# Optimization experiments

Hardware: AMD Instinct MI355X
Metric: run time of the kernel (lower is better)

The kernel has to match this reference:

```python
import jax, jax.numpy as jnp
import numpy as np

B, S, D_IN = 2, 2048, 2048
H, G, HD = 16, 4, 128          # heads, kv groups, head_dim
GS = H // G                    # group size (heads per kv group)
EPS = 1e-6
SCALE = HD ** -0.5


def rms_norm(x, w):
    # RMSNorm over last dim (head_dim)
    var = jnp.mean(jnp.square(x), axis=-1, keepdims=True)
    return x * jax.lax.rsqrt(var + EPS) * w


def apply_rope(x, cos, sin):
    # x: [b, h, s, d]; cos/sin: [s, d]. Rotate-half convention.
    d = x.shape[-1]
    x1, x2 = x[..., : d // 2], x[..., d // 2 :]
    rotated = jnp.concatenate([-x2, x1], axis=-1)
    return x * cos[None, None] + rotated * sin[None, None]


def setup_inputs() -> dict:
    key = jax.random.key(0)
    ks = jax.random.split(key, 8)
    x = jax.random.normal(ks[0], (B, S, D_IN), jnp.float32)
    mask = jnp.triu(jnp.ones((S, S), jnp.bool_), k=1)  # True = masked (future)
    # realistic RoPE tables
    inv_freq = 1.0 / (10000.0 ** (jnp.arange(0, HD, 2, dtype=jnp.float32) / HD))
    angles = jnp.arange(S, dtype=jnp.float32)[:, None] * inv_freq[None, :]  # [S, HD/2]
    angles = jnp.concatenate([angles, angles], axis=-1)  # [S, HD]
    cos, sin = jnp.cos(angles), jnp.sin(angles)
    sd = 0.02
    Wq = jax.random.normal(ks[1], (D_IN, H * HD), jnp.float32) * sd
    Wk = jax.random.normal(ks[2], (D_IN, G * HD), jnp.float32) * sd
    Wv = jax.random.normal(ks[3], (D_IN, G * HD), jnp.float32) * sd
    Wo = jax.random.normal(ks[4], (H * HD, D_IN), jnp.float32) * sd
    q_norm_w = jnp.ones((HD,), jnp.float32)
    k_norm_w = jnp.ones((HD,), jnp.float32)
    return {"x": x, "mask": mask, "cos": cos, "sin": sin, "Wq": Wq, "Wk": Wk,
            "Wv": Wv, "Wo": Wo, "q_norm_w": q_norm_w, "k_norm_w": k_norm_w}


def reference(x, mask, cos, sin, Wq, Wk, Wv, Wo, q_norm_w, k_norm_w):
    b, s, _ = x.shape
    q = (x @ Wq).reshape(b, s, H, HD).transpose(0, 2, 1, 3)   # [b,H,s,d]
    k = (x @ Wk).reshape(b, s, G, HD).transpose(0, 2, 1, 3)   # [b,G,s,d]
    v = (x @ Wv).reshape(b, s, G, HD).transpose(0, 2, 1, 3)   # [b,G,s,d]
    q = rms_norm(q, q_norm_w)
    k = rms_norm(k, k_norm_w)
    q = apply_rope(q, cos, sin)
    k = apply_rope(k, cos, sin)
    q = q * SCALE
    # GQA without materializing repeated KV: split heads into [G, GS]
    qg = q.reshape(b, G, GS, s, HD)                           # [b,G,gs,s,d]
    scores = jnp.einsum('bghsd,bgtd->bghst', qg, k)           # [b,G,gs,s,s]
    scores = jnp.where(mask[None, None, None], -jnp.inf, scores)
    attn = jax.nn.softmax(scores, axis=-1)
    ctx = jnp.einsum('bghst,bgtd->bghsd', attn, v)            # [b,G,gs,s,d]
    ctx = ctx.reshape(b, H, s, HD).transpose(0, 2, 1, 3).reshape(b, s, H * HD)
    return ctx @ Wo
```

## Files before the change

### kernel.cpp

```cpp
#include <hip/hip_runtime.h>
#include <cstdint>
#include <cstddef>

typedef unsigned short u16;
typedef __bf16 bf16x8 __attribute__((ext_vector_type(8)));
typedef float f32x4 __attribute__((ext_vector_type(4)));

#define SLEN 2048
#define NHEADS 16
#define NGRP 4

__device__ inline float bf2f(u16 u) { return __uint_as_float(((unsigned)u) << 16); }
__device__ inline u16 f2bf(float f) {
    unsigned u = __float_as_uint(f);
    u += 0x7fffu + ((u >> 16) & 1u);
    return (u16)(u >> 16);
}

__device__ inline f32x4 mfma16(bf16x8 a, bf16x8 b, f32x4 c) {
    return __builtin_amdgcn_mfma_f32_16x16x32_bf16(a, b, c, 0, 0, 0);
}

__device__ inline void memfence_compiler() { __asm__ volatile("" ::: "memory"); }

__device__ inline void cp16(const u16* g, u16* l) {
    __builtin_amdgcn_global_load_lds(
        (__attribute__((address_space(1))) void*)(u16*)g,
        (__attribute__((address_space(3))) void*)l, 16, 0, 0);
}


__device__ inline void transpose_f32_body(u16 (*tile)[65], const float* __restrict__ in,
                                          u16* __restrict__ out, int R, int C, int bx, int by,
                                          int tid) {
    const long r0 = (long)by * 64, c0 = (long)bx * 64;
    for (int j = 0; j < 4; j++) {
        int c = j * 256 + tid;
        int lr = c >> 4, lc = (c & 15) * 4;
        float4 v = *(const float4*)&in[(r0 + lr) * (long)C + c0 + lc];
        tile[lr][lc + 0] = f2bf(v.x); tile[lr][lc + 1] = f2bf(v.y);
        tile[lr][lc + 2] = f2bf(v.z); tile[lr][lc + 3] = f2bf(v.w);
    }
    __syncthreads();
    for (int j = 0; j < 4; j++) {
        int c = j * 256 + tid;
        int orow = c >> 4, oc = (c & 15) * 4;
        ushort4 vv;
        vv.x = tile[oc + 0][orow]; vv.y = tile[oc + 1][orow];
        vv.z = tile[oc + 2][orow]; vv.w = tile[oc + 3][orow];
        *(ushort4*)&out[(c0 + orow) * (long)R + r0 + oc] = vv;
    }
}

__device__ inline void transpose_bf_body(u16 (*tile)[65], const u16* __restrict__ in, long inRS,
                                         u16* __restrict__ out, int R, int C, int bx, int by,
                                         int tid) {
    const long r0 = (long)by * 64, c0 = (long)bx * 64;
    for (int j = 0; j < 4; j++) {
        int c = j * 256 + tid;
        int lr = c >> 4, lc = (c & 15) * 4;
        ushort4 vv = *(const ushort4*)&in[(r0 + lr) * inRS + c0 + lc];
        tile[lr][lc + 0] = vv.x; tile[lr][lc + 1] = vv.y;
        tile[lr][lc + 2] = vv.z; tile[lr][lc + 3] = vv.w;
    }
    __syncthreads();
    for (int j = 0; j < 4; j++) {
        int c = j * 256 + tid;
        int orow = c >> 4, oc = (c & 15) * 4;
        ushort4 vv;
        vv.x = tile[oc + 0][orow]; vv.y = tile[oc + 1][orow];
        vv.z = tile[oc + 2][orow]; vv.w = tile[oc + 3][orow];
        *(ushort4*)&out[(c0 + orow) * (long)R + r0 + oc] = vv;
    }
}

__device__ inline void normrope_body(u16* __restrict__ buf, long rowstride, int heads,
                                     const u16* __restrict__ w,
                                     const float* __restrict__ cosf, const float* __restrict__ sinf,
                                     float scale, int row, int lane) {
    u16* p = buf + (long)(row / heads) * rowstride + (row % heads) * 128;
    float x1 = bf2f(p[lane]);
    float x2 = bf2f(p[lane + 64]);
    float ss = x1 * x1 + x2 * x2;
    for (int off = 1; off < 64; off <<= 1) ss += __shfl_xor(ss, off);
    float inv = rsqrtf(ss * (1.f / 128.f) + 1e-6f);
    int s = (row / heads) % SLEN;
    float c1 = cosf[s * 128 + lane], c2 = cosf[s * 128 + 64 + lane];
    float s1 = sinf[s * 128 + lane], s2 = sinf[s * 128 + 64 + lane];
    float w1 = bf2f(w[lane]), w2 = bf2f(w[lane + 64]);
    float y1 = x1 * inv * w1, y2 = x2 * inv * w2;
    p[lane]      = f2bf((y1 * c1 - y2 * s1) * scale);
    p[lane + 64] = f2bf((y2 * c2 + y1 * s2) * scale);
}

__global__ __launch_bounds__(256) void prep_k(const float* __restrict__ x, u16* __restrict__ xbf,
                                              const float* __restrict__ qw, const float* __restrict__ kw,
                                              u16* qwb, u16* kwb,
                                              const float* __restrict__ Wq, const float* __restrict__ Wk,
                                              const float* __restrict__ Wv, u16* __restrict__ wqkvT) {
    __shared__ u16 tile[64][65];
    const int bid = blockIdx.x, tid = threadIdx.x;
    if (bid < 8192) {
        long i = ((long)bid * 256 + tid) * 4;
        float4 v = *(const float4*)(x + i);
        ushort4 o;
        o.x = f2bf(v.x); o.y = f2bf(v.y); o.z = f2bf(v.z); o.w = f2bf(v.w);
        *(ushort4*)(xbf + i) = o;
    } else if (bid == 8192) {
        if (tid < 128) qwb[tid] = f2bf(qw[tid]);
        else kwb[tid - 128] = f2bf(kw[tid - 128]);
    } else if (bid < 9217) {
        int rem = bid - 8193;
        transpose_f32_body(tile, Wq, wqkvT, 2048, 2048, rem & 31, rem >> 5, tid);
    } else if (bid < 9473) {
        int rem = bid - 9217;
        transpose_f32_body(tile, Wk, wqkvT + 2048L * 2048, 2048, 512, rem & 7, rem >> 3, tid);
    } else {
        int rem = bid - 9473;
        transpose_f32_body(tile, Wv, wqkvT + 2560L * 2048, 2048, 512, rem & 7, rem >> 3, tid);
    }
}

__global__ __launch_bounds__(256) void mid_k(u16* __restrict__ qkvb, u16* __restrict__ vTb,
                                             const u16* __restrict__ qwb, const u16* __restrict__ kwb,
                                             const float* __restrict__ cosf, const float* __restrict__ sinf,
                                             const float* __restrict__ Wo, u16* __restrict__ woT) {
    __shared__ u16 tile[64][65];
    const int bid = blockIdx.x, tid = threadIdx.x;
    if (bid < 512) {
        transpose_bf_body(tile, qkvb + 2560, 3072L, vTb, 4096, 512, bid & 7, bid >> 3, tid);
    } else if (bid < 16896) {
        int row = (bid - 512) * 4 + (tid >> 6);
        normrope_body(qkvb, 3072L, NHEADS, qwb, cosf, sinf, 0.08838834764831845f, row, tid & 63);
    } else if (bid < 20992) {
        int row = (bid - 16896) * 4 + (tid >> 6);
        normrope_body(qkvb + 2048, 3072L, NGRP, kwb, cosf, sinf, 1.0f, row, tid & 63);
    } else {
        int rem = bid - 20992;
        transpose_f32_body(tile, Wo, woT, 2048, 2048, rem & 31, rem >> 5, tid);
    }
}

template <typename OutT, int MQ>
__global__ __launch_bounds__(512, 2) void gemm256(const u16* __restrict__ A, const u16* __restrict__ Bt,
                                                  OutT* __restrict__ C, int N, int K) {
    extern __shared__ u16 smem[];
    const int tid = threadIdx.x;
    const int lane = tid & 63, wave = tid >> 6;
    const int l15 = lane & 15, quad = lane >> 4;
    const int wm = (wave >> 2) * (MQ * 64), wn = (wave & 3) * 64;
    const long m0 = (long)blockIdx.y * (MQ * 128), n0 = (long)blockIdx.x * 256;

    constexpr int ASZ = MQ * 8192;

    f32x4 acc[MQ * 4][4];
    #pragma unroll
    for (int i = 0; i < MQ * 4; i++)
        #pragma unroll
        for (int j = 0; j < 4; j++) acc[i][j] = {0.f, 0.f, 0.f, 0.f};

    const int sn = wave * 64 + lane;
    const u16* aBase = A + m0 * (long)K;
    const u16* bBase = Bt + n0 * (long)K;

    auto stage = [&](int kt, int p) {
        u16* al = smem + p * ASZ + wave * 512;
        u16* bl = smem + 2 * ASZ + p * 16384 + wave * 512;
        #pragma unroll
        for (int j = 0; j < MQ * 2; j++) {
            int n = j * 512 + sn;
            int r = n >> 3;
            int c = (n & 7) ^ (r & 7);
            cp16(aBase + (long)r * K + kt + c * 8, al + j * 4096);
        }
        #pragma unroll
        for (int j = 0; j < 4; j++) {
            int n = j * 512 + sn;
            int r = n >> 3;
            int c = (n & 7) ^ (r & 7);
            cp16(bBase + (long)r * K + kt + c * 8, bl + j * 4096);
        }
    };

    stage(0, 0);
    const int nkt = K >> 6;

    for (int t = 0; t < nkt; ++t) {
        const int cur = t & 1;
        if (t + 1 < nkt) {
            stage((t + 1) << 6, cur ^ 1);
            if constexpr (MQ == 2) asm volatile("s_waitcnt vmcnt(8)" ::: "memory");
            else                   asm volatile("s_waitcnt vmcnt(6)" ::: "memory");
        } else {
            asm volatile("s_waitcnt vmcnt(0)" ::: "memory");
        }
        __builtin_amdgcn_s_barrier();

        const u16* asb = smem + cur * ASZ;
        const u16* bsb = smem + 2 * ASZ + cur * 16384;

        bf16x8 bfr[4][2];
        #pragma unroll
        for (int ni = 0; ni < 4; ni++) {
            const int row = wn + ni * 16 + l15;
            #pragma unroll
            for (int ks = 0; ks < 2; ks++)
                bfr[ni][ks] = *(const bf16x8*)&bsb[row * 64 + (((ks << 2) + quad) ^ (row & 7)) * 8];
        }
        #pragma unroll
        for (int mq = 0; mq < MQ; mq++) {
            bf16x8 af[4][2];
            #pragma unroll
            for (int mi = 0; mi < 4; mi++) {
                const int row = wm + mq * 64 + mi * 16 + l15;
                #pragma unroll
                for (int ks = 0; ks < 2; ks++)
                    af[mi][ks] = *(const bf16x8*)&asb[row * 64 + (((ks << 2) + quad) ^ (row & 7)) * 8];
            }
            #pragma unroll
            for (int mi = 0; mi < 4; mi++)
                #pragma unroll
                for (int ni = 0; ni < 4; ni++) {
                    f32x4 v = acc[mq * 4 + mi][ni];
                    v = mfma16(af[mi][0], bfr[ni][0], v);
                    v = mfma16(af[mi][1], bfr[ni][1], v);
                    acc[mq * 4 + mi][ni] = v;
                }
        }
        __builtin_amdgcn_s_barrier();
    }

    #pragma unroll
    for (int mi = 0; mi < MQ * 4; mi++)
        #pragma unroll
        for (int r = 0; r < 4; r++) {
            long row = m0 + wm + mi * 16 + quad * 4 + r;
            OutT* crow = C + row * (long)N + n0 + wn + l15;
            #pragma unroll
            for (int ni = 0; ni < 4; ni++) {
                float v = acc[mi][ni][r];
                if constexpr (sizeof(OutT) == 2) crow[ni * 16] = f2bf(v);
                else crow[ni * 16] = v;
            }
        }
}

__global__ __launch_bounds__(256, 2) void attn(const u16* __restrict__ qkv, const u16* __restrict__ vT,
                                               u16* __restrict__ ctx) {
    __shared__ u16 KB[64 * 128];
    __shared__ u16 VB[128 * 64];
    __shared__ u16 Ps[4][2][16][72];
    __shared__ float Al[4][2][16];
    const int tid = threadIdx.x;
    const int lane = tid & 63, wave = tid >> 6;
    const int l15 = lane & 15, quad = lane >> 4;
    const int bg = blockIdx.x & 7, b = bg >> 2, g = bg & 3;
    const int rest = blockIdx.x >> 3;
    const int h = g * 4 + (rest & 3);
    const int idx = rest >> 2;
    const int qt = (idx < 8) ? (15 - idx) : (idx - 8);
    const int wr = qt * 128 + wave * 32;

    union { bf16x8 v; u16 s[8]; } uo;
    for (int j = 0; j < 8; j++) uo.s[j] = 0x3F80;
    const bf16x8 ones = uo.v;

    bf16x8 qa[2][4];
    for (int m = 0; m < 2; m++) {
        const u16* qp = qkv + (long)(b * SLEN + wr + m * 16 + l15) * 3072 + h * 128 + quad * 8;
        for (int kc = 0; kc < 4; kc++) qa[m][kc] = *(const bf16x8*)(qp + kc * 32);
    }
    float m_i[2] = {-__builtin_inff(), -__builtin_inff()};
    f32x4 l_acc[2];
    f32x4 o[2][8];
    for (int m = 0; m < 2; m++) l_acc[m] = {0.f, 0.f, 0.f, 0.f};
    for (int m = 0; m < 2; m++)
        for (int nf = 0; nf < 8; nf++) o[m][nf] = {0.f, 0.f, 0.f, 0.f};

    const u16* kqb = qkv + (long)b * SLEN * 3072 + 2048 + g * 128;
    const u16* vgb = vT + (long)g * 128 * 4096 + (long)b * SLEN;
    const int xk = (l15 & 7) << 4;
    const int nt = 2 * qt + 2;

    for (int t = 0; t < nt; ++t) {
        const int t0 = t * 64;
        #pragma unroll
        for (int i = 0; i < 4; ++i) {
            const int j = wave * 4 + i;
            {
                const int row = j * 4 + (lane >> 4);
                const int cs = lane & 15;
                cp16(kqb + (long)(t0 + row) * 3072 + ((cs ^ (row & 7)) * 8), &KB[j * 512]);
            }
            {
                const int row = j * 8 + (lane >> 3);
                const int cs = lane & 7;
                cp16(vgb + (long)row * 4096 + t0 + ((cs ^ (row & 7)) * 8), &VB[j * 512]);
            }
        }
        __syncthreads();

        if (t0 <= wr + 31) {
            bf16x8 kf[4][4];
            #pragma unroll
            for (int nf = 0; nf < 4; nf++)
                #pragma unroll
                for (int kc = 0; kc < 4; kc++)
                    kf[nf][kc] = *(const bf16x8*)((const char*)KB +
                                  (nf * 16 + l15) * 256 + ((quad * 16 + kc * 64) ^ xk));

            f32x4 sc[2][4];
            for (int m = 0; m < 2; m++)
                for (int nf = 0; nf < 4; nf++) sc[m][nf] = {0.f, 0.f, 0.f, 0.f};
            #pragma unroll
            for (int kc = 0; kc < 4; kc++)
                #pragma unroll
                for (int nf = 0; nf < 4; nf++) {
                    sc[0][nf] = mfma16(kf[nf][kc], qa[0][kc], sc[0][nf]);
                    sc[1][nf] = mfma16(kf[nf][kc], qa[1][kc], sc[1][nf]);
                }
            if (t0 + 63 > wr) {
                #pragma unroll
                for (int m = 0; m < 2; m++) {
                    int qrow = wr + m * 16 + l15;
                    #pragma unroll
                    for (int nf = 0; nf < 4; nf++)
                        #pragma unroll
                        for (int r = 0; r < 4; r++)
                            if (t0 + nf * 16 + quad * 4 + r > qrow) sc[m][nf][r] = -__builtin_inff();
                }
            }
            float alpha[2];
            #pragma unroll
            for (int m = 0; m < 2; m++) {
                float mx = sc[m][0][0];
                #pragma unroll
                for (int nf = 0; nf < 4; nf++)
                    #pragma unroll
                    for (int r = 0; r < 4; r++) mx = fmaxf(mx, sc[m][nf][r]);
                mx = fmaxf(mx, __shfl_xor(mx, 16));
                mx = fmaxf(mx, __shfl_xor(mx, 32));
                float mn = fmaxf(m_i[m], mx);
                alpha[m] = __expf(m_i[m] - mn);
                m_i[m] = mn;
                Al[wave][m][l15] = alpha[m];
            }
            #pragma unroll
            for (int m = 0; m < 2; m++)
                #pragma unroll
                for (int nf = 0; nf < 4; nf++) {
                    ushort4 pk;
                    pk.x = f2bf(__expf(sc[m][nf][0] - m_i[m]));
                    pk.y = f2bf(__expf(sc[m][nf][1] - m_i[m]));
                    pk.z = f2bf(__expf(sc[m][nf][2] - m_i[m]));
                    pk.w = f2bf(__expf(sc[m][nf][3] - m_i[m]));
                    *(ushort4*)&Ps[wave][m][l15][nf * 16 + quad * 4] = pk;
                }
            memfence_compiler();
            f32x4 al[2];
            al[0] = *(const f32x4*)&Al[wave][0][quad * 4];
            al[1] = *(const f32x4*)&Al[wave][1][quad * 4];
            #pragma unroll
            for (int m = 0; m < 2; m++) {
                #pragma unroll
                for (int nf = 0; nf < 8; nf++)
                    #pragma unroll
                    for (int r = 0; r < 4; r++) o[m][nf][r] *= al[m][r];
                #pragma unroll
                for (int r = 0; r < 4; r++) l_acc[m][r] *= al[m][r];
            }
            {
                bf16x8 vf[8];
                #pragma unroll
                for (int nf = 0; nf < 8; nf++)
                    vf[nf] = *(const bf16x8*)((const char*)VB +
                              (nf * 16 + l15) * 128 + ((quad * 16) ^ xk));
                bf16x8 pa0 = *(const bf16x8*)&Ps[wave][0][l15][quad * 8];
                bf16x8 pa1 = *(const bf16x8*)&Ps[wave][1][l15][quad * 8];
                #pragma unroll
                for (int nf = 0; nf < 8; nf++) {
                    o[0][nf] = mfma16(pa0, vf[nf], o[0][nf]);
                    o[1][nf] = mfma16(pa1, vf[nf], o[1][nf]);
                }
                l_acc[0] = mfma16(pa0, ones, l_acc[0]);
                l_acc[1] = mfma16(pa1, ones, l_acc[1]);
            }
            {
                bf16x8 vf[8];
                #pragma unroll
                for (int nf = 0; nf < 8; nf++)
                    vf[nf] = *(const bf16x8*)((const char*)VB +
                              (nf * 16 + l15) * 128 + ((64 + quad * 16) ^ xk));
                bf16x8 pa0 = *(const bf16x8*)&Ps[wave][0][l15][32 + quad * 8];
                bf16x8 pa1 = *(const bf16x8*)&Ps[wave][1][l15][32 + quad * 8];
                #pragma unroll
                for (int nf = 0; nf < 8; nf++) {
                    o[0][nf] = mfma16(pa0, vf[nf], o[0][nf]);
                    o[1][nf] = mfma16(pa1, vf[nf], o[1][nf]);
                }
                l_acc[0] = mfma16(pa0, ones, l_acc[0]);
                l_acc[1] = mfma16(pa1, ones, l_acc[1]);
            }
            memfence_compiler();
        }
        __syncthreads();
    }

    #pragma unroll
    for (int m = 0; m < 2; m++)
        #pragma unroll
        for (int r = 0; r < 4; r++) {
            float inv = 1.f / l_acc[m][r];
            int srow = wr + m * 16 + quad * 4 + r;
            u16* cp = ctx + (long)(b * SLEN + srow) * 2048 + h * 128 + l15;
            #pragma unroll
            for (int nf = 0; nf < 8; nf++) cp[nf * 16] = f2bf(o[m][nf][r] * inv);
        }
}

extern "C" void kernel_launch(void* const* d_in, const int* in_sizes, int n_in,
                              void* d_out, int out_size, void* d_ws, size_t ws_size,
                              hipStream_t stream) {
    const float* x    = (const float*)d_in[0];
    const float* cosi = (const float*)d_in[2];
    const float* sini = (const float*)d_in[3];
    const float* Wq   = (const float*)d_in[4];
    const float* Wk   = (const float*)d_in[5];
    const float* Wv   = (const float*)d_in[6];
    const float* Wo   = (const float*)d_in[7];
    const float* qw   = (const float*)d_in[8];
    const float* kw   = (const float*)d_in[9];
    float* out = (float*)d_out;
    char* ws = (char*)d_ws;

    const size_t MB = 1 << 20;
    u16* qkvb  = (u16*)(ws);
    u16* vTb   = (u16*)(ws + 24 * MB);
    u16* xbf   = (u16*)(ws + 28 * MB);
    u16* ctx   = (u16*)(ws + 28 * MB);
    u16* wqkvT = (u16*)(ws + 44 * MB);
    u16* woT   = (u16*)(ws + 44 * MB);
    u16* qwb   = (u16*)(ws + 56 * MB);
    u16* kwb   = (u16*)(ws + 56 * MB + 256);

    prep_k<<<9729, 256, 0, stream>>>(x, xbf, qw, kw, qwb, kwb, Wq, Wk, Wv, wqkvT);

    gemm256<u16, 2><<<dim3(12, 16), 512, 131072, stream>>>(xbf, wqkvT, qkvb, 3072, 2048);

    mid_k<<<22016, 256, 0, stream>>>(qkvb, vTb, qwb, kwb, cosi, sini, Wo, woT);

    attn<<<dim3(512, 1, 1), 256, 0, stream>>>(qkvb, vTb, ctx);

    gemm256<float, 1><<<dim3(8, 32), 512, 98304, stream>>>(ctx, woT, out, 2048, 2048);
}
```

Before: 320.2 us.

## Restructure GEMM into finer-grained eight-phase pipeline with interleaved loads and MFMA

Replaces the double-buffered 64-wide K-step GEMM with a version that splits each K tile into two 32-wide halves and each half into two M sub-phases. Each sub-phase issues part of the next tile's global-to-LDS copies before the MFMA burst, and raises wave priority around the MFMAs. Tile shapes also change: the output-projection GEMM now uses 256x128 tiles instead of 128x256. The aim is to overlap memory traffic with matrix math and cut per-step stalls, at the cost of more barriers per K tile and new swizzle and wait-count logic that has to be exactly right.

```diff
diff --git a/kernel.cpp b/kernel.cpp
--- a/kernel.cpp
+++ b/kernel.cpp
@@ -141,103 +141,120 @@
     }
 }
 
-template <typename OutT, int MQ>
-__global__ __launch_bounds__(512, 2) void gemm256(const u16* __restrict__ A, const u16* __restrict__ Bt,
-                                                  OutT* __restrict__ C, int N, int K) {
+template <typename OutT, int NI>
+__global__ __launch_bounds__(512, 2) void gemm8p(const u16* __restrict__ A, const u16* __restrict__ Bt,
+                                                 OutT* __restrict__ C, int N, int K) {
     extern __shared__ u16 smem[];
+    constexpr int AUNIT = 8192;
+    constexpr int BUNIT = NI * 2048;
+    constexpr int GATE = 2 + NI / 2;
     const int tid = threadIdx.x;
     const int lane = tid & 63, wave = tid >> 6;
     const int l15 = lane & 15, quad = lane >> 4;
-    const int wm = (wave >> 2) * (MQ * 64), wn = (wave & 3) * 64;
-    const long m0 = (long)blockIdx.y * (MQ * 128), n0 = (long)blockIdx.x * 256;
-
-    constexpr int ASZ = MQ * 8192;
-
-    f32x4 acc[MQ * 4][4];
+    const int wm = (wave >> 2) * 128, wn = (wave & 3) * (NI * 16);
+    const long m0 = (long)blockIdx.y * 256, n0 = (long)blockIdx.x * (NI * 64);
+
+    f32x4 acc[8][NI];
     #pragma unroll
-    for (int i = 0; i < MQ * 4; i++)
-        #pragma unroll
-        for (int j = 0; j < 4; j++) acc[i][j] = {0.f, 0.f, 0.f, 0.f};
-
-    const int sn = wave * 64 + lane;
+    for (int i = 0; i < 8; i++)
+        #pragma unroll
+        for (int j = 0; j < NI; j++) acc[i][j] = {0.f, 0.f, 0.f, 0.f};
+
     const u16* aBase = A + m0 * (long)K;
     const u16* bBase = Bt + n0 * (long)K;
 
-    auto stage = [&](int kt, int p) {
-        u16* al = smem + p * ASZ + wave * 512;
-        u16* bl = smem + 2 * ASZ + p * 16384 + wave * 512;
-        #pragma unroll
-        for (int j = 0; j < MQ * 2; j++) {
-            int n = j * 512 + sn;
-            int r = n >> 3;
-            int c = (n & 7) ^ (r & 7);
-            cp16(aBase + (long)r * K + kt + c * 8, al + j * 4096);
-        }
-        #pragma unroll
-        for (int j = 0; j < 4; j++) {
-            int n = j * 512 + sn;
-            int r = n >> 3;
-            int c = (n & 7) ^ (r & 7);
-            cp16(bBase + (long)r * K + kt + c * 8, bl + j * 4096);
+    auto stageA = [&](int kt, int c, int k) {
+        u16* dst = smem + (c * 2 + k) * AUNIT + wave * 512;
+        #pragma unroll
+        for (int i = 0; i < 2; i++) {
+            int cd = i * 512 + wave * 64 + lane;
+            int r = cd >> 2;
+            int js = (cd & 3) ^ ((r >> 1) & 3);
+            cp16(aBase + (long)r * K + kt + k * 32 + js * 8, dst + i * 4096);
         }
     };
-
-    stage(0, 0);
+    auto stageB = [&](int kt, int c, int k) {
+        u16* dst = smem + 4 * AUNIT + (c * 2 + k) * BUNIT + wave * 512;
+        #pragma unroll
+        for (int i = 0; i < NI / 2; i++) {
+            int cd = i * 512 + wave * 64 + lane;
+            int r = cd >> 2;
+            int js = (cd & 3) ^ ((r >> 1) & 3);
+            cp16(bBase + (long)r * K + kt + k * 32 + js * 8, dst + i * 4096);
+        }
+    };
+
+    stageA(0, 0, 0); stageB(0, 0, 0); stageA(0, 0, 1); stageB(0, 0, 1);
+
     const int nkt = K >> 6;
 
     for (int t = 0; t < nkt; ++t) {
-        const int cur = t & 1;
-        if (t + 1 < nkt) {
-            stage((t + 1) << 6, cur ^ 1);
-            if constexpr (MQ == 2) asm volatile("s_waitcnt vmcnt(8)" ::: "memory");
-            else                   asm volatile("s_waitcnt vmcnt(6)" ::: "memory");
-        } else {
-            asm volatile("s_waitcnt vmcnt(0)" ::: "memory");
-        }
-        __builtin_amdgcn_s_barrier();
-
-        const u16* asb = smem + cur * ASZ;
-        const u16* bsb = smem + 2 * ASZ + cur * 16384;
-
-        bf16x8 bfr[4][2];
-        #pragma unroll
-        for (int ni = 0; ni < 4; ni++) {
-            const int row = wn + ni * 16 + l15;
-            #pragma unroll
-            for (int ks = 0; ks < 2; ks++)
-                bfr[ni][ks] = *(const bf16x8*)&bsb[row * 64 + (((ks << 2) + quad) ^ (row & 7)) * 8];
-        }
-        #pragma unroll
-        for (int mq = 0; mq < MQ; mq++) {
-            bf16x8 af[4][2];
+        const int c = t & 1;
+        const int kt1 = (t + 1) << 6;
+        const bool more = (t + 1) < nkt;
+        #pragma unroll
+        for (int k = 0; k < 2; ++k) {
+            if (k == 0 || more) {
+                if constexpr (NI == 4) asm volatile("s_waitcnt vmcnt(4)" ::: "memory");
+                else                   asm volatile("s_waitcnt vmcnt(3)" ::: "memory");
+            } else {
+                asm volatile("s_waitcnt vmcnt(0)" ::: "memory");
+            }
+            __builtin_amdgcn_s_barrier();
+
+            const u16* au = smem + (c * 2 + k) * AUNIT;
+            const u16* bu = smem + 4 * AUNIT + (c * 2 + k) * BUNIT;
+
+            bf16x8 bfr[NI], af[4];
+            #pragma unroll
+            for (int ni = 0; ni < NI; ni++) {
+                const int r = wn + ni * 16 + l15;
+                bfr[ni] = *(const bf16x8*)&bu[r * 32 + (quad ^ ((r >> 1) & 3)) * 8];
+            }
             #pragma unroll
             for (int mi = 0; mi < 4; mi++) {
-                const int row = wm + mq * 64 + mi * 16 + l15;
-                #pragma unroll
-                for (int ks = 0; ks < 2; ks++)
-                    af[mi][ks] = *(const bf16x8*)&asb[row * 64 + (((ks << 2) + quad) ^ (row & 7)) * 8];
-            }
+                const int r = wm + mi * 16 + l15;
+                af[mi] = *(const bf16x8*)&au[r * 32 + (quad ^ ((r >> 1) & 3)) * 8];
+            }
+            if (more) stageA(kt1, c ^ 1, k);
+            asm volatile("s_waitcnt lgkmcnt(0)" ::: "memory");
+            __builtin_amdgcn_sched_barrier(0);
+            __builtin_amdgcn_s_setprio(1);
             #pragma unroll
             for (int mi = 0; mi < 4; mi++)
                 #pragma unroll
-                for (int ni = 0; ni < 4; ni++) {
-                    f32x4 v = acc[mq * 4 + mi][ni];
-                    v = mfma16(af[mi][0], bfr[ni][0], v);
-                    v = mfma16(af[mi][1], bfr[ni][1], v);
-                    acc[mq * 4 + mi][ni] = v;
-                }
-        }
-        __builtin_amdgcn_s_barrier();
+                for (int ni = 0; ni < NI; ni++)
+                    acc[mi][ni] = mfma16(af[mi], bfr[ni], acc[mi][ni]);
+            __builtin_amdgcn_s_setprio(0);
+            __builtin_amdgcn_s_barrier();
+
+            #pragma unroll
+            for (int mi = 0; mi < 4; mi++) {
+                const int r = wm + 64 + mi * 16 + l15;
+                af[mi] = *(const bf16x8*)&au[r * 32 + (quad ^ ((r >> 1) & 3)) * 8];
+            }
+            if (more) stageB(kt1, c ^ 1, k);
+            asm volatile("s_waitcnt lgkmcnt(0)" ::: "memory");
+            __builtin_amdgcn_sched_barrier(0);
+            __builtin_amdgcn_s_setprio(1);
+            #pragma unroll
+            for (int mi = 0; mi < 4; mi++)
+                #pragma unroll
+                for (int ni = 0; ni < NI; ni++)
+                    acc[4 + mi][ni] = mfma16(af[mi], bfr[ni], acc[4 + mi][ni]);
+            __builtin_amdgcn_s_setprio(0);
+            __builtin_amdgcn_s_barrier();
+        }
     }
 
     #pragma unroll
-    for (int mi = 0; mi < MQ * 4; mi++)
+    for (int mi = 0; mi < 8; mi++)
         #pragma unroll
         for (int r = 0; r < 4; r++) {
             long row = m0 + wm + mi * 16 + quad * 4 + r;
             OutT* crow = C + row * (long)N + n0 + wn + l15;
             #pragma unroll
-            for (int ni = 0; ni < 4; ni++) {
+            for (int ni = 0; ni < NI; ni++) {
                 float v = acc[mi][ni][r];
                 if constexpr (sizeof(OutT) == 2) crow[ni * 16] = f2bf(v);
                 else crow[ni * 16] = v;
@@ -445,11 +462,11 @@
 
     prep_k<<<9729, 256, 0, stream>>>(x, xbf, qw, kw, qwb, kwb, Wq, Wk, Wv, wqkvT);
 
-    gemm256<u16, 2><<<dim3(12, 16), 512, 131072, stream>>>(xbf, wqkvT, qkvb, 3072, 2048);
+    gemm8p<u16, 4><<<dim3(12, 16), 512, 131072, stream>>>(xbf, wqkvT, qkvb, 3072, 2048);
 
     mid_k<<<22016, 256, 0, stream>>>(qkvb, vTb, qwb, kwb, cosi, sini, Wo, woT);
 
     attn<<<dim3(512, 1, 1), 256, 0, stream>>>(qkvb, vTb, ctx);
 
-    gemm256<float, 1><<<dim3(8, 32), 512, 98304, stream>>>(ctx, woT, out, 2048, 2048);
-}
+    gemm8p<float, 2><<<dim3(16, 16), 512, 98304, stream>>>(ctx, woT, out, 2048, 2048);
+}
```

New measurement: 320.2 us. About the same (+0.0%).
